# Optimization experiments

Measured on AMD Instinct MI355X. Metric: run time of the kernel, lower is better.

The kernel has to match this reference:

```python
import jax, jax.numpy as jnp
import numpy as np

N = 50000      # nodes
E = 500000     # edges (avg degree 10)
G = 64         # graphs (events)
IN = 7
H = 64
EPS = 1e-5


def setup_inputs() -> dict:
    key = jax.random.key(0)
    ks = iter(jax.random.split(key, 64))
    d = {}
    d["x"] = jax.random.normal(next(ks), (N, IN), jnp.float32)
    d["edge_index"] = jax.random.randint(next(ks), (2, E), 0, N, dtype=jnp.int32)
    d["batch"] = jnp.sort(jax.random.randint(next(ks), (N,), 0, G, dtype=jnp.int32))
    dims = [(IN, H), (H, 2 * H), (2 * H, 4 * H)]
    for i, (ic, oc) in enumerate(dims, 1):
        d[f"b{i}_W1"] = jax.random.normal(next(ks), (2 * ic, oc), jnp.float32) * 0.05
        d[f"b{i}_b1"] = jnp.zeros((oc,), jnp.float32)
        d[f"b{i}_g1"] = jnp.ones((oc,), jnp.float32)
        d[f"b{i}_beta1"] = jnp.zeros((oc,), jnp.float32)
        d[f"b{i}_W2"] = jax.random.normal(next(ks), (oc, oc), jnp.float32) * 0.05
        d[f"b{i}_b2"] = jnp.zeros((oc,), jnp.float32)
        d[f"b{i}_g2"] = jnp.ones((oc,), jnp.float32)
        d[f"b{i}_beta2"] = jnp.zeros((oc,), jnp.float32)
    d["head_W1"] = jax.random.normal(next(ks), (4 * H, 2 * H), jnp.float32) * 0.05
    d["head_b1"] = jnp.zeros((2 * H,), jnp.float32)
    d["head_W2"] = jax.random.normal(next(ks), (2 * H, 2), jnp.float32) * 0.05
    d["head_b2"] = jnp.zeros((2,), jnp.float32)
    return d


def _bn(h, g, b):
    # BatchNorm1d in training mode: batch statistics over edge dim
    m = h.mean(axis=0)
    v = h.var(axis=0)
    return (h - m) * jax.lax.rsqrt(v + EPS) * g + b


def _edgeconv(x, src, dst, W1, b1, g1, be1, W2, b2, g2, be2):
    # PyG EdgeConv: message = MLP(cat[x_i, x_j - x_i]), aggregated at target i=dst
    xi = x[dst]                                   # [E, C]
    xj = x[src]                                   # [E, C]
    e = jnp.concatenate([xi, xj - xi], axis=-1)   # [E, 2C]
    h = jax.nn.relu(_bn(e @ W1 + b1, g1, be1))
    h = jax.nn.relu(_bn(h @ W2 + b2, g2, be2))
    s = jax.ops.segment_sum(h, dst, num_segments=N)
    cnt = jax.ops.segment_sum(jnp.ones((h.shape[0],), h.dtype), dst, num_segments=N)
    return s / jnp.maximum(cnt, 1.0)[:, None]     # mean aggregation


def reference(x, edge_index, batch,
              b1_W1, b1_b1, b1_g1, b1_beta1, b1_W2, b1_b2, b1_g2, b1_beta2,
              b2_W1, b2_b1, b2_g1, b2_beta1, b2_W2, b2_b2, b2_g2, b2_beta2,
              b3_W1, b3_b1, b3_g1, b3_beta1, b3_W2, b3_b2, b3_g2, b3_beta2,
              head_W1, head_b1, head_W2, head_b2):
    src, dst = edge_index[0], edge_index[1]
    h = _edgeconv(x, src, dst, b1_W1, b1_b1, b1_g1, b1_beta1, b1_W2, b1_b2, b1_g2, b1_beta2)
    h = _edgeconv(h, src, dst, b2_W1, b2_b1, b2_g1, b2_beta1, b2_W2, b2_b2, b2_g2, b2_beta2)
    h = _edgeconv(h, src, dst, b3_W1, b3_b1, b3_g1, b3_beta1, b3_W2, b3_b2, b3_g2, b3_beta2)
    # global mean pool per graph
    s = jax.ops.segment_sum(h, batch, num_segments=G)
    cnt = jax.ops.segment_sum(jnp.ones((N,), h.dtype), batch, num_segments=G)
    g = s / jnp.maximum(cnt, 1.0)[:, None]        # [G, 256]
    # head (dropout is identity in eval)
    z = jax.nn.relu(g @ head_W1 + head_b1)
    return z @ head_W2 + head_b2                  # [G, 2]
```

## Files before the change

kernel.cpp:

```cpp
#include <hip/hip_runtime.h>
#include <stdint.h>

constexpr int NN = 50000;
constexpr int NE = 500000;
constexpr int NG = 64;
constexpr float BN_EPS = 1e-5f;

typedef __attribute__((ext_vector_type(8))) short bf16x8;
typedef __attribute__((ext_vector_type(4))) float f32x4;

__device__ inline float bf2f(unsigned short u) {
    return __uint_as_float(((unsigned int)u) << 16);
}
__device__ inline unsigned short f2bf_rne(float f) {
    unsigned int u = __float_as_uint(f);
    unsigned int r = (u + 0x7fffu + ((u >> 16) & 1u)) >> 16;
    return (unsigned short)r;
}

template<int CPT> __device__ inline void load_row(const float* p, float* o) {
    if constexpr (CPT == 2) { float2 v = *(const float2*)p; o[0]=v.x; o[1]=v.y; }
    else if constexpr (CPT == 4) { float4 v = *(const float4*)p; o[0]=v.x; o[1]=v.y; o[2]=v.z; o[3]=v.w; }
    else { load_row<4>(p, o); load_row<4>(p+4, o+4); }
}
template<int CPT> __device__ inline void store_row(float* p, const float* v) {
    if constexpr (CPT == 2) { *(float2*)p = make_float2(v[0], v[1]); }
    else if constexpr (CPT == 4) { *(float4*)p = make_float4(v[0], v[1], v[2], v[3]); }
    else { store_row<4>(p, v); store_row<4>(p+4, v+4); }
}

__global__ void k_zero16(uint4* p, int n) {
    int i = blockIdx.x * 256 + threadIdx.x;
    if (i < n) p[i] = uint4{0u, 0u, 0u, 0u};
}

__global__ void k_diag(float* out, int n, float val) {
    int i = blockIdx.x * 256 + threadIdx.x;
    if (i < n) out[i] = val;
}

__global__ void k_deg(const int* __restrict__ dst, int* __restrict__ degi) {
    int e = blockIdx.x * 256 + threadIdx.x;
    if (e < NE) atomicAdd(&degi[dst[e]], 1);
}

__global__ void k_scan(const int* __restrict__ degi, int* __restrict__ rowptr) {
    __shared__ int buf[1024];
    __shared__ int carry_s;
    const int tid = threadIdx.x;
    if (tid == 0) carry_s = 0;
    __syncthreads();
    for (int base = 0; base < NN; base += 1024) {
        int i = base + tid;
        int v = (i < NN) ? degi[i] : 0;
        buf[tid] = v;
        __syncthreads();
        for (int off = 1; off < 1024; off <<= 1) {
            int t = (tid >= off) ? buf[tid - off] : 0;
            __syncthreads();
            buf[tid] += t;
            __syncthreads();
        }
        if (i < NN) rowptr[i] = carry_s + buf[tid] - v;
        __syncthreads();
        if (tid == 0) carry_s += buf[1023];
        __syncthreads();
    }
    if (tid == 0) rowptr[NN] = carry_s;
}

__global__ void k_fill(const int* __restrict__ dst, const int* __restrict__ rowptr,
                       int* __restrict__ cursor, int* __restrict__ eidx) {
    int e = blockIdx.x * 256 + threadIdx.x;
    if (e < NE) {
        int d = dst[e];
        int p = atomicAdd(&cursor[d], 1);
        eidx[rowptr[d] + p] = e;
    }
}

__global__ void k_grange(const int* __restrict__ batch, int* __restrict__ gse) {
    int n = blockIdx.x * 256 + threadIdx.x;
    if (n >= NN) return;
    int b = batch[n];
    if (n == 0 || batch[n-1] != b) gse[b] = n;
    if (n == NN-1 || batch[n+1] != b) gse[NG + b] = n + 1;
}

template<int OC>
__global__ void k_bnfin(const float* __restrict__ st, const float* __restrict__ g,
                        const float* __restrict__ be, float* __restrict__ dv) {
    int c = threadIdx.x;
    const float invE = 1.0f / (float)NE;
    float m = st[c] * invE;
    float v = st[OC + c] * invE - m * m;
    float sc = g[c] * rsqrtf(v + BN_EPS);
    dv[c] = sc;
    dv[OC + c] = be[c] - m * sc;
}

template<int OC>
__global__ void k_packW(const float* __restrict__ W,
                        unsigned short* __restrict__ Wph, unsigned short* __restrict__ Wpl) {
    constexpr int NT = OC / 16;
    const int l = threadIdx.x;
    const int ktnt = blockIdx.x;
    const int n = (ktnt % NT) * 16 + (l & 15);
    const int kbase = (ktnt / NT) * 32 + (l >> 4) * 8;
    size_t fo = ((size_t)ktnt * 64 + l) * 8;
    #pragma unroll
    for (int b = 0; b < 8; b++) {
        float w = W[(size_t)(kbase + b) * OC + n];
        unsigned short h = f2bf_rne(w);
        Wph[fo + b] = h;
        Wpl[fo + b] = f2bf_rne(w - bf2f(h));
    }
}

template<int CIN, int OC>
__global__ __launch_bounds__(256) void k_nodeproj(
    const float* __restrict__ x, const float* __restrict__ W1,
    const float* __restrict__ b1, float* __restrict__ A, float* __restrict__ Bn)
{
    constexpr int SP = CIN + 1;
    constexpr int CPT = OC / 32;
    __shared__ float xs[32 * SP];
    const int t = threadIdx.x;
    const int n0 = blockIdx.x * 32;
    {
        const int el = t >> 3, l8 = t & 7;
        int n = n0 + el; if (n >= NN) n = NN - 1;
        const float* xp = x + (size_t)n * CIN;
        for (int k = l8; k < CIN; k += 8) xs[el * SP + k] = xp[k];
    }
    __syncthreads();
    const int tx = t & 31, ty = t >> 5;
    float accA[4][CPT], accB[4][CPT];
    #pragma unroll
    for (int i = 0; i < 4; i++)
        #pragma unroll
        for (int j = 0; j < CPT; j++) { accA[i][j] = 0.f; accB[i][j] = 0.f; }

    const float* Wa = W1 + tx * CPT;
    const float* Wb = W1 + (size_t)CIN * OC + tx * CPT;
    for (int k = 0; k < CIN; k++) {
        float wa[CPT], wb[CPT];
        load_row<CPT>(Wa + (size_t)k * OC, wa);
        load_row<CPT>(Wb + (size_t)k * OC, wb);
        #pragma unroll
        for (int i = 0; i < 4; i++) {
            float ev = xs[(ty * 4 + i) * SP + k];
            #pragma unroll
            for (int j = 0; j < CPT; j++) {
                accA[i][j] = fmaf(ev, wa[j] - wb[j], accA[i][j]);
                accB[i][j] = fmaf(ev, wb[j], accB[i][j]);
            }
        }
    }
    float bs[CPT];
    load_row<CPT>(b1 + tx * CPT, bs);
    #pragma unroll
    for (int i = 0; i < 4; i++) {
        const int n = n0 + ty * 4 + i;
        if (n < NN) {
            float va[CPT];
            #pragma unroll
            for (int j = 0; j < CPT; j++) va[j] = accA[i][j] + bs[j];
            store_row<CPT>(A  + (size_t)n * OC + tx * CPT, va);
            store_row<CPT>(Bn + (size_t)n * OC + tx * CPT, accB[i]);
        }
    }
}

template<int OC>
__global__ __launch_bounds__(256) void k_stats1(
    const float* __restrict__ A, const float* __restrict__ Bn,
    const int* __restrict__ src, const int* __restrict__ dst,
    const int* __restrict__ eidx, float* __restrict__ stats)
{
    constexpr int CPT = OC / 32;
    __shared__ float reds[4 * OC];
    __shared__ float redq[4 * OC];
    const int t = threadIdx.x;
    const int l32 = t & 31, grp = t >> 5;
    float s[CPT], q[CPT];
    #pragma unroll
    for (int j = 0; j < CPT; j++) { s[j] = 0.f; q[j] = 0.f; }
    for (int i = blockIdx.x * 8 + grp; i < NE; i += 8192) {
        const int e = eidx[i];
        float av[CPT], bv[CPT];
        load_row<CPT>(A  + (size_t)dst[e] * OC + l32 * CPT, av);
        load_row<CPT>(Bn + (size_t)src[e] * OC + l32 * CPT, bv);
        #pragma unroll
        for (int j = 0; j < CPT; j++) {
            float h = av[j] + bv[j];
            s[j] += h; q[j] += h * h;
        }
    }
    #pragma unroll
    for (int j = 0; j < CPT; j++) {
        s[j] += __shfl_down(s[j], 32);
        q[j] += __shfl_down(q[j], 32);
    }
    const int w = t >> 6, lane = t & 63;
    if (lane < 32) {
        #pragma unroll
        for (int j = 0; j < CPT; j++) {
            reds[w * OC + lane * CPT + j] = s[j];
            redq[w * OC + lane * CPT + j] = q[j];
        }
    }
    __syncthreads();
    for (int c = t; c < OC; c += 256) {
        float S = reds[c] + reds[OC + c] + reds[2 * OC + c] + reds[3 * OC + c];
        float Q = redq[c] + redq[OC + c] + redq[2 * OC + c] + redq[3 * OC + c];
        atomicAdd(&stats[c], S);
        atomicAdd(&stats[OC + c], Q);
    }
}

template<int OC, int MODE>
__global__ __launch_bounds__(256, 2) void k_efuse(
    const float* __restrict__ A, const float* __restrict__ Bn,
    const int* __restrict__ src, const int* __restrict__ dst,
    const int* __restrict__ eidx,
    const unsigned short* __restrict__ Wph, const unsigned short* __restrict__ Wpl,
    const float* __restrict__ b2,
    const float* __restrict__ dv1, float* __restrict__ stats,
    const float* __restrict__ dv2, float* __restrict__ xout)
{
    constexpr int ETL = 128;
    constexpr int NT = OC / 16;
    constexpr int NTW = NT / 2;
    constexpr int NCH = OC / 64;
    constexpr int SROWS = 8192 / OC;
    constexpr int NSTRIP = ETL / SROWS;
    constexpr int YSTR = OC + 4;
    constexpr int YB = SROWS * YSTR * 4;
    constexpr int SMB = (MODE == 1 && YB > 32768) ? YB : 32768;

    __shared__ __align__(16) unsigned char smem[SMB];
    __shared__ int sdst_s[ETL], ssrc_s[ETL];

    const int t = threadIdx.x;
    const int e0 = blockIdx.x * ETL;
    const int valid = (NE - e0 < ETL) ? (NE - e0) : ETL;

    if (t < ETL) {
        int dn = -1, sn = -1;
        if (t < valid) { int e = eidx[e0 + t]; dn = dst[e]; sn = src[e]; }
        sdst_s[t] = dn; ssrc_s[t] = sn;
    }
    __syncthreads();

    const int lane = t & 63, wave = t >> 6;
    const int rg = wave >> 1, ch = wave & 1;
    const int lr = lane & 15, lg = lane >> 4;

    f32x4 acc[4][NTW];
    #pragma unroll
    for (int m = 0; m < 4; m++)
        #pragma unroll
        for (int n = 0; n < NTW; n++) acc[m][n] = (f32x4){0.f, 0.f, 0.f, 0.f};

    const int brow = t >> 1, bhf = t & 1;

    for (int kc = 0; kc < NCH; kc++) {
        {
            const int gc0 = kc * 64 + bhf * 32;
            if (brow < valid) {
                const float* Ar  = A  + (size_t)sdst_s[brow] * OC + gc0;
                const float* Br  = Bn + (size_t)ssrc_s[brow] * OC + gc0;
                const float* scp = dv1 + gc0;
                const float* shp = dv1 + OC + gc0;
                #pragma unroll
                for (int i = 0; i < 8; i++) {
                    float4 a  = *(const float4*)(Ar + i * 4);
                    float4 b  = *(const float4*)(Br + i * 4);
                    float4 sc = *(const float4*)(scp + i * 4);
                    float4 sh = *(const float4*)(shp + i * 4);
                    float tv[4];
                    tv[0] = fmaxf(fmaf(a.x + b.x, sc.x, sh.x), 0.f);
                    tv[1] = fmaxf(fmaf(a.y + b.y, sc.y, sh.y), 0.f);
                    tv[2] = fmaxf(fmaf(a.z + b.z, sc.z, sh.z), 0.f);
                    tv[3] = fmaxf(fmaf(a.w + b.w, sc.w, sh.w), 0.f);
                    unsigned short hv[4], lv[4];
                    #pragma unroll
                    for (int j = 0; j < 4; j++) {
                        unsigned short h = f2bf_rne(tv[j]);
                        hv[j] = h;
                        lv[j] = f2bf_rne(tv[j] - bf2f(h));
                    }
                    const int byt = (brow * 128 + bhf * 64 + i * 8) ^ ((brow & 7) << 4);
                    *(ushort4*)(smem + byt) = *(ushort4*)hv;
                    *(ushort4*)(smem + 16384 + byt) = *(ushort4*)lv;
                }
            } else {
                const ushort4 z = ushort4{0, 0, 0, 0};
                #pragma unroll
                for (int i = 0; i < 8; i++) {
                    const int byt = (brow * 128 + bhf * 64 + i * 8) ^ ((brow & 7) << 4);
                    *(ushort4*)(smem + byt) = z;
                    *(ushort4*)(smem + 16384 + byt) = z;
                }
            }
        }
        __syncthreads();

        #pragma unroll
        for (int kt2 = 0; kt2 < 2; kt2++) {
            bf16x8 ah[4], al[4];
            #pragma unroll
            for (int m = 0; m < 4; m++) {
                const int r = rg * 64 + m * 16 + lr;
                const int byt = (r * 128 + kt2 * 64 + lg * 16) ^ ((r & 7) << 4);
                ah[m] = *(const bf16x8*)(smem + byt);
                al[m] = *(const bf16x8*)(smem + 16384 + byt);
            }
            #pragma unroll
            for (int n = 0; n < NTW; n++) {
                const size_t fo = ((size_t)((kc * 2 + kt2) * NT + ch * NTW + n) * 64 + lane) * 8;
                bf16x8 wh = *(const bf16x8*)(Wph + fo);
                bf16x8 wl = *(const bf16x8*)(Wpl + fo);
                #pragma unroll
                for (int m = 0; m < 4; m++) {
                    acc[m][n] = __builtin_amdgcn_mfma_f32_16x16x32_bf16(ah[m], wh, acc[m][n], 0, 0, 0);
                    acc[m][n] = __builtin_amdgcn_mfma_f32_16x16x32_bf16(ah[m], wl, acc[m][n], 0, 0, 0);
                    acc[m][n] = __builtin_amdgcn_mfma_f32_16x16x32_bf16(al[m], wh, acc[m][n], 0, 0, 0);
                }
            }
        }
        __syncthreads();
    }

    if constexpr (MODE == 0) {
        #pragma unroll
        for (int n = 0; n < NTW; n++) {
            const int col = ch * (OC / 2) + n * 16 + lr;
            const float bb = b2[col];
            float s = 0.f, q = 0.f;
            #pragma unroll
            for (int m = 0; m < 4; m++) {
                const int rbase = rg * 64 + m * 16 + lg * 4;
                #pragma unroll
                for (int e = 0; e < 4; e++) {
                    float h = (rbase + e < valid) ? (acc[m][n][e] + bb) : 0.f;
                    s += h; q += h * h;
                }
            }
            s += __shfl_xor(s, 16); s += __shfl_xor(s, 32);
            q += __shfl_xor(q, 16); q += __shfl_xor(q, 32);
            if (lg == 0) {
                atomicAdd(&stats[col], s);
                atomicAdd(&stats[OC + col], q);
            }
        }
    } else {
        float* yt = (float*)smem;
        const int acol = t % OC;
        const int aseg = t / OC;
        #pragma unroll
        for (int s = 0; s < NSTRIP; s++) {
            const int r0 = s * SROWS;
            #pragma unroll
            for (int m = 0; m < 4; m++) {
                const int base = rg * 64 + m * 16;
                if (base >= r0 && base < r0 + SROWS) {
                    #pragma unroll
                    for (int n = 0; n < NTW; n++) {
                        const int col = ch * (OC / 2) + n * 16 + lr;
                        const float bb = b2[col], scv = dv2[col], shv = dv2[OC + col];
                        #pragma unroll
                        for (int e = 0; e < 4; e++) {
                            const int rl = base - r0 + lg * 4 + e;
                            yt[rl * YSTR + col] = fmaxf(fmaf(acc[m][n][e] + bb, scv, shv), 0.f);
                        }
                    }
                }
            }
            __syncthreads();
            {
                const int rbeg = aseg * 32;
                float a = 0.f; int cur = -1;
                for (int r = 0; r < 32; r++) {
                    const int gr = r0 + rbeg + r;
                    if (gr >= valid) break;
                    const int nd = sdst_s[gr];
                    if (nd != cur) {
                        if (cur >= 0) atomicAdd(&xout[(size_t)cur * OC + acol], a);
                        cur = nd; a = 0.f;
                    }
                    a += yt[(rbeg + r) * YSTR + acol];
                }
                if (cur >= 0) atomicAdd(&xout[(size_t)cur * OC + acol], a);
            }
            __syncthreads();
        }
    }
}

template<int OC>
__global__ __launch_bounds__(256) void k_div(float* __restrict__ xout,
                                             const int* __restrict__ degi) {
    constexpr int CPT = OC / 32;
    const int tx = threadIdx.x & 31;
    const int n = blockIdx.x * 8 + (threadIdx.x >> 5);
    if (n >= NN) return;
    const float inv = 1.0f / fmaxf((float)degi[n], 1.0f);
    float v[CPT];
    load_row<CPT>(xout + (size_t)n * OC + tx * CPT, v);
    #pragma unroll
    for (int j = 0; j < CPT; j++) v[j] *= inv;
    store_row<CPT>(xout + (size_t)n * OC + tx * CPT, v);
}

__global__ void k_pool(const float* __restrict__ x3, const int* __restrict__ gse,
                       float* __restrict__ pooled) {
    const int g = blockIdx.x, c = threadIdx.x;
    const int beg = gse[g], end = gse[NG + g];
    float s = 0.f;
    for (int n = beg; n < end; n++) s += x3[(size_t)n * 256 + c];
    pooled[g * 256 + c] = s / fmaxf((float)(end - beg), 1.0f);
}

__global__ void k_head(const float* __restrict__ pooled,
                       const float* __restrict__ W1, const float* __restrict__ b1,
                       const float* __restrict__ W2, const float* __restrict__ b2,
                       float* __restrict__ out) {
    __shared__ float gv[256];
    __shared__ float z[128];
    const int g = blockIdx.x;
    gv[threadIdx.x] = pooled[g * 256 + threadIdx.x];
    __syncthreads();
    if (threadIdx.x < 128) {
        const int c = threadIdx.x;
        float s = b1[c];
        for (int k = 0; k < 256; k++) s = fmaf(gv[k], W1[k * 128 + c], s);
        z[c] = fmaxf(s, 0.f);
    }
    __syncthreads();
    if (threadIdx.x < 2) {
        const int o = threadIdx.x;
        float s = b2[o];
        for (int k = 0; k < 128; k++) s = fmaf(z[k], W2[k * 2 + o], s);
        out[g * 2 + o] = s;
    }
}

template<int CIN, int OC>
static void run_block(const float* xin, const float* const* Q,
                      float* A, float* B, const int* src, const int* dst,
                      const int* eidx, const unsigned short* Wph, const unsigned short* Wpl,
                      float* st, float* dv, const int* degi,
                      float* xout, hipStream_t s)
{
    const int EG = (NE + 127) / 128;
    k_nodeproj<CIN, OC><<<(NN + 31) / 32, 256, 0, s>>>(xin, Q[0], Q[1], A, B);
    k_stats1<OC><<<1024, 256, 0, s>>>(A, B, src, dst, eidx, st);
    k_bnfin<OC><<<1, OC, 0, s>>>(st, Q[2], Q[3], dv);
    k_efuse<OC, 0><<<EG, 256, 0, s>>>(A, B, src, dst, eidx, Wph, Wpl, Q[5], dv, st + 512, nullptr, nullptr);
    k_bnfin<OC><<<1, OC, 0, s>>>(st + 512, Q[6], Q[7], dv + 512);
    k_zero16<<<((NN * OC / 4) + 255) / 256, 256, 0, s>>>((uint4*)xout, NN * OC / 4);
    k_efuse<OC, 1><<<EG, 256, 0, s>>>(A, B, src, dst, eidx, Wph, Wpl, Q[5], dv, nullptr, dv + 512, xout);
    k_div<OC><<<(NN + 7) / 8, 256, 0, s>>>(xout, degi);
}

extern "C" void kernel_launch(void* const* d_in, const int* in_sizes, int n_in,
                              void* d_out, int out_size, void* d_ws, size_t ws_size,
                              hipStream_t stream)
{
    (void)in_sizes; (void)n_in;
    const float* x = (const float*)d_in[0];
    const int* ei = (const int*)d_in[1];
    const int* src = ei;
    const int* dst = ei + NE;
    const int* batch = (const int*)d_in[2];
    const float* P[28];
    for (int i = 0; i < 28; i++) P[i] = (const float*)d_in[3 + i];
    float* out = (float*)d_out;

    size_t offs[18];
    {
        size_t o = 0;
        auto take = [&](size_t bytes) -> size_t {
            size_t r = o; o = (o + bytes + 255) & ~(size_t)255; return r;
        };
        offs[0] = take((size_t)NN * 256 * 4);
        offs[1] = take((size_t)NN * 256 * 4);
        offs[2] = take((size_t)NN * 256 * 4);
        offs[3] = take((size_t)NN * 128 * 4);
        offs[4] = o;
        offs[5] = take((size_t)NN * 4);
        offs[6] = take((size_t)NN * 4);
        offs[7] = take(3 * 1024 * 4);
        offs[8] = take(2 * NG * 4);
        offs[9] = o;
        offs[10] = take((size_t)(NN + 1) * 4);
        offs[11] = take((size_t)NE * 4);
        offs[12] = take(3 * 1024 * 4);
        offs[13] = take((size_t)NG * 256 * 4);
        offs[14] = take((64*64 + 128*128 + 256*256) * 2);
        offs[15] = take((64*64 + 128*128 + 256*256) * 2);
        offs[16] = o;
        if (ws_size < o) {
            float val = 1000.0f + (float)(ws_size >> 20);
            k_diag<<<(out_size + 255) / 256, 256, 0, stream>>>(out, out_size, val);
            return;
        }
    }

    char* W = (char*)d_ws;
    float* A  = (float*)(W + offs[0]);
    float* B  = (float*)(W + offs[1]);
    float* xa = (float*)(W + offs[2]);
    float* xb = (float*)(W + offs[3]);
    int* degi = (int*)(W + offs[5]);
    int* cursor = (int*)(W + offs[6]);
    float* stats = (float*)(W + offs[7]);
    int* gse = (int*)(W + offs[8]);
    int* rowptr = (int*)(W + offs[10]);
    int* eidx = (int*)(W + offs[11]);
    float* dv = (float*)(W + offs[12]);
    float* pooled = (float*)(W + offs[13]);
    unsigned short* Wph = (unsigned short*)(W + offs[14]);
    unsigned short* Wpl = (unsigned short*)(W + offs[15]);
    unsigned short* Wph1 = Wph,            * Wpl1 = Wpl;
    unsigned short* Wph2 = Wph + 64*64,    * Wpl2 = Wpl + 64*64;
    unsigned short* Wph3 = Wph2 + 128*128, * Wpl3 = Wpl2 + 128*128;

    int nz = (int)((offs[9] - offs[4]) / 16);
    k_zero16<<<(nz + 255) / 256, 256, 0, stream>>>((uint4*)(W + offs[4]), nz);

    k_deg<<<(NE + 255) / 256, 256, 0, stream>>>(dst, degi);
    k_scan<<<1, 1024, 0, stream>>>(degi, rowptr);
    k_fill<<<(NE + 255) / 256, 256, 0, stream>>>(dst, rowptr, cursor, eidx);
    k_grange<<<(NN + 255) / 256, 256, 0, stream>>>(batch, gse);

    k_packW<64> <<<(64/32)*(64/16),   64, 0, stream>>>(P[4],  Wph1, Wpl1);
    k_packW<128><<<(128/32)*(128/16), 64, 0, stream>>>(P[12], Wph2, Wpl2);
    k_packW<256><<<(256/32)*(256/16), 64, 0, stream>>>(P[20], Wph3, Wpl3);

    run_block<7,   64>(x,  P + 0,  A, B, src, dst, eidx, Wph1, Wpl1, stats + 0,    dv + 0,    degi, xa, stream);
    run_block<64, 128>(xa, P + 8,  A, B, src, dst, eidx, Wph2, Wpl2, stats + 1024, dv + 1024, degi, xb, stream);
    run_block<128,256>(xb, P + 16, A, B, src, dst, eidx, Wph3, Wpl3, stats + 2048, dv + 2048, degi, xa, stream);

    k_pool<<<NG, 256, 0, stream>>>(xa, gse, pooled);
    k_head<<<NG, 256, 0, stream>>>(pooled, P[24], P[25], P[26], P[27], out);
}
```

Before: 2.704 ms.

## Use single-bf16 MFMA in stats pass and prefetch gathered rows across k-chunks

In MODE 0 (the pass that only gathers BN statistics), the split-bf16 three-product MFMA is replaced by a single bf16 product, which drops the low-part LDS buffer and the extra weight loads. Separately, the gathered A/B rows for the next k-chunk are now loaded into registers while the current chunk's MFMAs run. This cuts MFMA work and LDS use in the stats pass and hides gather latency. The cost is lower precision in the batch statistics and more register pressure from the prefetch buffers.

```diff
diff --git a/kernel.cpp b/kernel.cpp
--- a/kernel.cpp
+++ b/kernel.cpp
@@ -237,7 +237,8 @@
     constexpr int NSTRIP = ETL / SROWS;
     constexpr int YSTR = OC + 4;
     constexpr int YB = SROWS * YSTR * 4;
-    constexpr int SMB = (MODE == 1 && YB > 32768) ? YB : 32768;
+    constexpr int TB = (MODE == 0) ? 16384 : 32768;
+    constexpr int SMB = (MODE == 1 && YB > TB) ? YB : TB;
 
     __shared__ __align__(16) unsigned char smem[SMB];
     __shared__ int sdst_s[ETL], ssrc_s[ETL];
@@ -264,36 +265,45 @@
         for (int n = 0; n < NTW; n++) acc[m][n] = (f32x4){0.f, 0.f, 0.f, 0.f};
 
     const int brow = t >> 1, bhf = t & 1;
+    const bool rvalid = (brow < valid);
+    const float* Arow = rvalid ? (A  + (size_t)sdst_s[brow] * OC + bhf * 32) : nullptr;
+    const float* Brow = rvalid ? (Bn + (size_t)ssrc_s[brow] * OC + bhf * 32) : nullptr;
+
+    float4 pa[8], pb[8];
+    if (rvalid) {
+        #pragma unroll
+        for (int i = 0; i < 8; i++) {
+            pa[i] = *(const float4*)(Arow + i * 4);
+            pb[i] = *(const float4*)(Brow + i * 4);
+        }
+    }
 
     for (int kc = 0; kc < NCH; kc++) {
         {
             const int gc0 = kc * 64 + bhf * 32;
-            if (brow < valid) {
-                const float* Ar  = A  + (size_t)sdst_s[brow] * OC + gc0;
-                const float* Br  = Bn + (size_t)ssrc_s[brow] * OC + gc0;
-                const float* scp = dv1 + gc0;
-                const float* shp = dv1 + OC + gc0;
+            if (rvalid) {
                 #pragma unroll
                 for (int i = 0; i < 8; i++) {
-                    float4 a  = *(const float4*)(Ar + i * 4);
-                    float4 b  = *(const float4*)(Br + i * 4);
-                    float4 sc = *(const float4*)(scp + i * 4);
-                    float4 sh = *(const float4*)(shp + i * 4);
+                    float4 a  = pa[i];
+                    float4 b  = pb[i];
+                    float4 sc = *(const float4*)(dv1 + gc0 + i * 4);
+                    float4 sh = *(const float4*)(dv1 + OC + gc0 + i * 4);
                     float tv[4];
                     tv[0] = fmaxf(fmaf(a.x + b.x, sc.x, sh.x), 0.f);
                     tv[1] = fmaxf(fmaf(a.y + b.y, sc.y, sh.y), 0.f);
                     tv[2] = fmaxf(fmaf(a.z + b.z, sc.z, sh.z), 0.f);
                     tv[3] = fmaxf(fmaf(a.w + b.w, sc.w, sh.w), 0.f);
-                    unsigned short hv[4], lv[4];
+                    unsigned short hv[4];
                     #pragma unroll
-                    for (int j = 0; j < 4; j++) {
-                        unsigned short h = f2bf_rne(tv[j]);
-                        hv[j] = h;
-                        lv[j] = f2bf_rne(tv[j] - bf2f(h));
-                    }
+                    for (int j = 0; j < 4; j++) hv[j] = f2bf_rne(tv[j]);
                     const int byt = (brow * 128 + bhf * 64 + i * 8) ^ ((brow & 7) << 4);
                     *(ushort4*)(smem + byt) = *(ushort4*)hv;
-                    *(ushort4*)(smem + 16384 + byt) = *(ushort4*)lv;
+                    if constexpr (MODE == 1) {
+                        unsigned short lv[4];
+                        #pragma unroll
+                        for (int j = 0; j < 4; j++) lv[j] = f2bf_rne(tv[j] - bf2f(hv[j]));
+                        *(ushort4*)(smem + 16384 + byt) = *(ushort4*)lv;
+                    }
                 }
             } else {
                 const ushort4 z = ushort4{0, 0, 0, 0};
@@ -301,11 +311,20 @@
                 for (int i = 0; i < 8; i++) {
                     const int byt = (brow * 128 + bhf * 64 + i * 8) ^ ((brow & 7) << 4);
                     *(ushort4*)(smem + byt) = z;
-                    *(ushort4*)(smem + 16384 + byt) = z;
+                    if constexpr (MODE == 1) *(ushort4*)(smem + 16384 + byt) = z;
                 }
             }
         }
         __syncthreads();
+
+        if (kc + 1 < NCH && rvalid) {
+            const int goff = (kc + 1) * 64;
+            #pragma unroll
+            for (int i = 0; i < 8; i++) {
+                pa[i] = *(const float4*)(Arow + goff + i * 4);
+                pb[i] = *(const float4*)(Brow + goff + i * 4);
+            }
+        }
 
         #pragma unroll
         for (int kt2 = 0; kt2 < 2; kt2++) {
@@ -315,18 +334,24 @@
                 const int r = rg * 64 + m * 16 + lr;
                 const int byt = (r * 128 + kt2 * 64 + lg * 16) ^ ((r & 7) << 4);
                 ah[m] = *(const bf16x8*)(smem + byt);
-                al[m] = *(const bf16x8*)(smem + 16384 + byt);
+                if constexpr (MODE == 1) al[m] = *(const bf16x8*)(smem + 16384 + byt);
             }
             #pragma unroll
             for (int n = 0; n < NTW; n++) {
                 const size_t fo = ((size_t)((kc * 2 + kt2) * NT + ch * NTW + n) * 64 + lane) * 8;
                 bf16x8 wh = *(const bf16x8*)(Wph + fo);
-                bf16x8 wl = *(const bf16x8*)(Wpl + fo);
-                #pragma unroll
-                for (int m = 0; m < 4; m++) {
-                    acc[m][n] = __builtin_amdgcn_mfma_f32_16x16x32_bf16(ah[m], wh, acc[m][n], 0, 0, 0);
-                    acc[m][n] = __builtin_amdgcn_mfma_f32_16x16x32_bf16(ah[m], wl, acc[m][n], 0, 0, 0);
-                    acc[m][n] = __builtin_amdgcn_mfma_f32_16x16x32_bf16(al[m], wh, acc[m][n], 0, 0, 0);
+                if constexpr (MODE == 0) {
+                    #pragma unroll
+                    for (int m = 0; m < 4; m++)
+                        acc[m][n] = __builtin_amdgcn_mfma_f32_16x16x32_bf16(ah[m], wh, acc[m][n], 0, 0, 0);
+                } else {
+                    bf16x8 wl = *(const bf16x8*)(Wpl + fo);
+                    #pragma unroll
+                    for (int m = 0; m < 4; m++) {
+                        acc[m][n] = __builtin_amdgcn_mfma_f32_16x16x32_bf16(ah[m], wh, acc[m][n], 0, 0, 0);
+                        acc[m][n] = __builtin_amdgcn_mfma_f32_16x16x32_bf16(ah[m], wl, acc[m][n], 0, 0, 0);
+                        acc[m][n] = __builtin_amdgcn_mfma_f32_16x16x32_bf16(al[m], wh, acc[m][n], 0, 0, 0);
+                    }
                 }
             }
         }
```

Result: slower. 2.862 ms (+5.8%).
